# Kernel optimization log

Hardware: AMD Instinct MI355X
Metric: run time of the kernel (lower is better)

## Reference

```python
import jax, jax.numpy as jnp
import numpy as np

# cfg constants (from init_kwargs)
RBF_START = 0.0
RBF_END = 10.0
RBF_STEPS = 32
ENERGY_SCALE = 1.0
EPS = 1e-10

L, R, E, F, P = 64, 4096, 32, 64, 8


def setup_inputs() -> dict:
    key = jax.random.key(0)
    ks = jax.random.split(key, 6)
    return {
        "lig_feat": jax.random.normal(ks[0], (L, E, F), dtype=jnp.float32),
        "rec_feat": jax.random.normal(ks[1], (R, E, F), dtype=jnp.float32),
        "lig_coords": jax.random.normal(ks[2], (P, L, 3), dtype=jnp.float32),
        "rec_coord": jax.random.normal(ks[3], (R, 3), dtype=jnp.float32),
        "weight": jax.random.normal(ks[4], (), dtype=jnp.float32),
        "bias": jax.random.normal(ks[5], (), dtype=jnp.float32),
    }


def reference(lig_feat, rec_feat, lig_coords, rec_coord, weight, bias):
    # attention coefficients: [L, R, E]
    atn = jnp.einsum('lef,ref->lre', lig_feat, rec_feat)
    mu = jnp.linspace(RBF_START, RBF_END, RBF_STEPS, dtype=jnp.float32)  # [E]
    sigma = (RBF_START - RBF_END) / RBF_STEPS

    def energy(lig_coord):  # lig_coord: [L, 3]
        # cdist_diff: eps added per-coordinate before sum, as in the torch code
        diff = lig_coord[:, None, :] - rec_coord[None, :, :]      # [L, R, 3]
        dists = jnp.sqrt(((diff * diff) + EPS).sum(-1))            # [L, R]
        z = (dists[..., None] - mu) / sigma                        # [L, R, E]
        rbfs = jnp.exp(-(z * z))
        return (atn * rbfs * ENERGY_SCALE).sum()

    Us = jax.vmap(energy)(lig_coords)  # [P]
    # ScaleOutput
    return Us * weight + bias
```

## Files before the change

### kernel.cpp

```cpp
#include <hip/hip_runtime.h>

#define NL 64
#define NR 4096
#define NE 32
#define NF 64
#define NP 8

#define DSCALE 3.8435917081166390f
#define MUSTEP 1.2398683f
#define EPS3   3e-10f

typedef _Float16 f16x8 __attribute__((ext_vector_type(8)));
typedef __fp16   h16x2 __attribute__((ext_vector_type(2)));
typedef float    f32x4 __attribute__((ext_vector_type(4)));

#define NBLK   2048
#define DS_TAB_BYTES (NL * NR * NP * 2)

__global__ __launch_bounds__(256)
void ff_dist(const float* __restrict__ lig_coords,
             const float* __restrict__ rec_coord,
             void* __restrict__ ws)
{
    const int tid = blockIdx.x * 256 + threadIdx.x;
    const int l = tid >> 12;
    const int r = tid & 4095;
    const float rx = rec_coord[r * 3 + 0];
    const float ry = rec_coord[r * 3 + 1];
    const float rz = rec_coord[r * 3 + 2];
    float d[NP];
#pragma unroll
    for (int p = 0; p < NP; ++p) {
        const float lx = lig_coords[(p * NL + l) * 3 + 0];
        const float ly = lig_coords[(p * NL + l) * 3 + 1];
        const float lz = lig_coords[(p * NL + l) * 3 + 2];
        const float dx = lx - rx, dy = ly - ry, dz = lz - rz;
        const float d2 = fmaf(dx, dx, fmaf(dy, dy, fmaf(dz, dz, EPS3)));
        d[p] = __builtin_amdgcn_sqrtf(d2) * DSCALE;
    }
    union { h16x2 h[4]; uint4 u; } pk;
#pragma unroll
    for (int q = 0; q < 4; ++q)
        pk.h[q] = __builtin_amdgcn_cvt_pkrtz(d[2 * q], d[2 * q + 1]);
    ((uint4*)ws)[tid] = pk.u;
}

__global__ __launch_bounds__(256, 4)
void ff_main(const float* __restrict__ lig_feat,
             const float* __restrict__ rec_feat,
             void* __restrict__ ws)
{
    __shared__ __align__(16) char recs[8192];
    __shared__ float wred[32];

    const int t    = threadIdx.x;
    const int bid  = blockIdx.x;
    const int rb   = bid & 255;
    const int eb   = bid >> 8;
    const int r0   = rb * 16;
    const int e0   = eb * 4;
    const int lane = t & 63;
    const int wv   = t >> 6;
    const int l0   = wv * 16;
    const int cn   = lane & 15;
    const int kg   = lane >> 4;

    const int srow = t >> 4, sf = (t & 15) * 4;
    const int swz = (8 * (t & 15)) ^ ((srow & 7) << 4);
#pragma unroll
    for (int e = 0; e < 4; ++e) {
        const float4 v = *(const float4*)&rec_feat[((r0 + srow) * NE + e0 + e) * NF + sf];
        union { h16x2 h[2]; uint2 u; } pk;
        pk.h[0] = __builtin_amdgcn_cvt_pkrtz(v.x, v.y);
        pk.h[1] = __builtin_amdgcn_cvt_pkrtz(v.z, v.w);
        *(uint2*)(recs + e * 2048 + srow * 128 + swz) = pk.u;
    }

    const uint4* dtab = (const uint4*)ws;
    float ds[4][NP];
#pragma unroll
    for (int reg = 0; reg < 4; ++reg) {
        union { uint4 u; _Float16 h[8]; } pk;
        pk.u = dtab[(l0 + kg * 4 + reg) * NR + r0 + cn];
#pragma unroll
        for (int p = 0; p < NP; ++p) ds[reg][p] = (float)pk.h[p];
    }

    __syncthreads();

    const int bsw = (cn & 7) << 4;
    const int b_row = cn * 128;
    const int b0o = b_row + ((kg * 16) ^ bsw);
    const int b1o = b_row + ((kg * 16 + 64) ^ bsw);
    const float* ligb = &lig_feat[((l0 + cn) * NE + e0) * NF + kg * 8];

    float U[NP];
#pragma unroll
    for (int p = 0; p < NP; ++p) U[p] = 0.f;

#pragma unroll
    for (int ee = 0; ee < 4; ++ee) {
        const float4 af0 = *(const float4*)(ligb + ee * NF + 0);
        const float4 af1 = *(const float4*)(ligb + ee * NF + 4);
        const float4 af2 = *(const float4*)(ligb + ee * NF + 32);
        const float4 af3 = *(const float4*)(ligb + ee * NF + 36);
        union { h16x2 h[4]; f16x8 v; } a0, a1;
        a0.h[0] = __builtin_amdgcn_cvt_pkrtz(af0.x, af0.y);
        a0.h[1] = __builtin_amdgcn_cvt_pkrtz(af0.z, af0.w);
        a0.h[2] = __builtin_amdgcn_cvt_pkrtz(af1.x, af1.y);
        a0.h[3] = __builtin_amdgcn_cvt_pkrtz(af1.z, af1.w);
        a1.h[0] = __builtin_amdgcn_cvt_pkrtz(af2.x, af2.y);
        a1.h[1] = __builtin_amdgcn_cvt_pkrtz(af2.z, af2.w);
        a1.h[2] = __builtin_amdgcn_cvt_pkrtz(af3.x, af3.y);
        a1.h[3] = __builtin_amdgcn_cvt_pkrtz(af3.z, af3.w);
        const f16x8 b0 = *(const f16x8*)(recs + ee * 2048 + b0o);
        const f16x8 b1 = *(const f16x8*)(recs + ee * 2048 + b1o);
        f32x4 C = {0.f, 0.f, 0.f, 0.f};
        C = __builtin_amdgcn_mfma_f32_16x16x32_f16(a0.v, b0, C, 0, 0, 0);
        C = __builtin_amdgcn_mfma_f32_16x16x32_f16(a1.v, b1, C, 0, 0, 0);

        const float mu = (float)(e0 + ee) * MUSTEP;
#pragma unroll
        for (int reg = 0; reg < 4; ++reg) {
            const float a = C[reg];
#pragma unroll
            for (int p = 0; p < NP; ++p) {
                const float z = ds[reg][p] - mu;
                U[p] = fmaf(a, __builtin_amdgcn_exp2f(-(z * z)), U[p]);
            }
        }
    }

#pragma unroll
    for (int p = 0; p < NP; ++p) {
        float v = U[p];
        for (int off = 32; off; off >>= 1) v += __shfl_down(v, off, 64);
        U[p] = v;
    }
    __syncthreads();
    if (lane == 0) {
#pragma unroll
        for (int p = 0; p < NP; ++p) wred[wv * 8 + p] = U[p];
    }
    __syncthreads();
    float* wsP = (float*)((char*)ws + DS_TAB_BYTES);
    if (t < NP)
        wsP[t * NBLK + bid] = wred[t] + wred[8 + t] + wred[16 + t] + wred[24 + t];
}

__global__ __launch_bounds__(512)
void ff_fin(const void* __restrict__ ws,
            const float* __restrict__ w,
            const float* __restrict__ b,
            float* __restrict__ out) {
    const float* wsP = (const float*)((const char*)ws + DS_TAB_BYTES);
    const int t = threadIdx.x, lane = t & 63, p = t >> 6;
    float s = 0.f;
#pragma unroll
    for (int j = 0; j < NBLK / 256; ++j) {
        const float4 v = *(const float4*)&wsP[p * NBLK + j * 256 + lane * 4];
        s += (v.x + v.y) + (v.z + v.w);
    }
    for (int off = 32; off; off >>= 1) s += __shfl_down(s, off, 64);
    if (lane == 0) out[p] = fmaf(s, w[0], b[0]);
}

extern "C" void kernel_launch(void* const* d_in, const int* in_sizes, int n_in,
                              void* d_out, int out_size, void* d_ws, size_t ws_size,
                              hipStream_t stream) {
    const float* lig_feat   = (const float*)d_in[0];
    const float* rec_feat   = (const float*)d_in[1];
    const float* lig_coords = (const float*)d_in[2];
    const float* rec_coord  = (const float*)d_in[3];
    const float* weight     = (const float*)d_in[4];
    const float* bias       = (const float*)d_in[5];
    float* out = (float*)d_out;

    hipLaunchKernelGGL(ff_dist, dim3(1024), dim3(256), 0, stream,
                       lig_coords, rec_coord, d_ws);
    hipLaunchKernelGGL(ff_main, dim3(NBLK), dim3(256), 0, stream,
                       lig_feat, rec_feat, d_ws);
    hipLaunchKernelGGL(ff_fin, dim3(1), dim3(512), 0, stream,
                       d_ws, weight, bias, out);
}
```

Measured before the change: 33.85 us.

## Fuse distance computation into main kernel and double per-block embedding tile

Removes the separate distance-table kernel. Each main block now computes its own 64x16x8 half-precision distance tile in shared memory from ligand coordinates staged in LDS and receptor coordinates read from global memory. Each block also covers 8 embedding channels instead of 4, which halves the grid to 1024 blocks and the number of times the distance tile is recomputed. This removes one launch and the 4 MB global round trip of the distance table, at the cost of redundant sqrt work per block and more shared memory, about 40 KB, which may limit occupancy.

```diff
diff --git a/kernel.cpp b/kernel.cpp
--- a/kernel.cpp
+++ b/kernel.cpp
@@ -14,84 +14,95 @@
 typedef __fp16   h16x2 __attribute__((ext_vector_type(2)));
 typedef float    f32x4 __attribute__((ext_vector_type(4)));
 
-#define NBLK   2048
-#define DS_TAB_BYTES (NL * NR * NP * 2)
+#define NBLK 1024
 
-__global__ __launch_bounds__(256)
-void ff_dist(const float* __restrict__ lig_coords,
-             const float* __restrict__ rec_coord,
-             void* __restrict__ ws)
-{
-    const int tid = blockIdx.x * 256 + threadIdx.x;
-    const int l = tid >> 12;
-    const int r = tid & 4095;
-    const float rx = rec_coord[r * 3 + 0];
-    const float ry = rec_coord[r * 3 + 1];
-    const float rz = rec_coord[r * 3 + 2];
-    float d[NP];
-#pragma unroll
-    for (int p = 0; p < NP; ++p) {
-        const float lx = lig_coords[(p * NL + l) * 3 + 0];
-        const float ly = lig_coords[(p * NL + l) * 3 + 1];
-        const float lz = lig_coords[(p * NL + l) * 3 + 2];
-        const float dx = lx - rx, dy = ly - ry, dz = lz - rz;
-        const float d2 = fmaf(dx, dx, fmaf(dy, dy, fmaf(dz, dz, EPS3)));
-        d[p] = __builtin_amdgcn_sqrtf(d2) * DSCALE;
-    }
-    union { h16x2 h[4]; uint4 u; } pk;
-#pragma unroll
-    for (int q = 0; q < 4; ++q)
-        pk.h[q] = __builtin_amdgcn_cvt_pkrtz(d[2 * q], d[2 * q + 1]);
-    ((uint4*)ws)[tid] = pk.u;
-}
+#define COORD_B 0
+#define DTAB_B  8192
+#define REC_B   24576
 
 __global__ __launch_bounds__(256, 4)
 void ff_main(const float* __restrict__ lig_feat,
              const float* __restrict__ rec_feat,
-             void* __restrict__ ws)
+             const float* __restrict__ lig_coords,
+             const float* __restrict__ rec_coord,
+             float* __restrict__ ws)
 {
-    __shared__ __align__(16) char recs[8192];
-    __shared__ float wred[32];
+    __shared__ __align__(16) char smem[40960];
 
     const int t    = threadIdx.x;
     const int bid  = blockIdx.x;
     const int rb   = bid & 255;
     const int eb   = bid >> 8;
     const int r0   = rb * 16;
-    const int e0   = eb * 4;
+    const int e0   = eb * 8;
     const int lane = t & 63;
     const int wv   = t >> 6;
     const int l0   = wv * 16;
     const int cn   = lane & 15;
     const int kg   = lane >> 4;
 
-    const int srow = t >> 4, sf = (t & 15) * 4;
-    const int swz = (8 * (t & 15)) ^ ((srow & 7) << 4);
 #pragma unroll
-    for (int e = 0; e < 4; ++e) {
-        const float4 v = *(const float4*)&rec_feat[((r0 + srow) * NE + e0 + e) * NF + sf];
+    for (int j = 0; j < 6; ++j) {
+        const int s = j * 256 + t;
+        const int p = s / 192;
+        const int rem = s - p * 192;
+        const int l = rem / 3, c = rem - l * 3;
+        *(float*)(smem + COORD_B + (l * 8 + p) * 16 + c * 4) = lig_coords[s];
+    }
+    const int srow = t >> 4, sfq = t & 15;
+    const int rswz = (8 * sfq) ^ ((srow & 7) << 4);
+#pragma unroll
+    for (int e = 0; e < 8; ++e) {
+        const float4 v = *(const float4*)&rec_feat[((r0 + srow) * NE + e0 + e) * NF + sfq * 4];
         union { h16x2 h[2]; uint2 u; } pk;
         pk.h[0] = __builtin_amdgcn_cvt_pkrtz(v.x, v.y);
         pk.h[1] = __builtin_amdgcn_cvt_pkrtz(v.z, v.w);
-        *(uint2*)(recs + e * 2048 + srow * 128 + swz) = pk.u;
+        *(uint2*)(smem + REC_B + e * 2048 + srow * 128 + rswz) = pk.u;
     }
+    __syncthreads();
 
-    const uint4* dtab = (const uint4*)ws;
+    {
+        const int bl = t >> 2;
+        const int br = t & 3;
+        float4 lp[NP];
+#pragma unroll
+        for (int p = 0; p < NP; ++p)
+            lp[p] = *(const float4*)(smem + COORD_B + (bl * 8 + p) * 16);
+#pragma unroll
+        for (int j = 0; j < 4; ++j) {
+            const int r = br + 4 * j;
+            const float rx = rec_coord[(r0 + r) * 3 + 0];
+            const float ry = rec_coord[(r0 + r) * 3 + 1];
+            const float rz = rec_coord[(r0 + r) * 3 + 2];
+            float d[NP];
+#pragma unroll
+            for (int p = 0; p < NP; ++p) {
+                const float dx = lp[p].x - rx, dy = lp[p].y - ry, dz = lp[p].z - rz;
+                const float d2 = fmaf(dx, dx, fmaf(dy, dy, fmaf(dz, dz, EPS3)));
+                d[p] = __builtin_amdgcn_sqrtf(d2) * DSCALE;
+            }
+            union { h16x2 h[4]; uint4 u; } pk;
+#pragma unroll
+            for (int q = 0; q < 4; ++q)
+                pk.h[q] = __builtin_amdgcn_cvt_pkrtz(d[2 * q], d[2 * q + 1]);
+            *(uint4*)(smem + DTAB_B + bl * 256 + ((r * 16) ^ ((bl & 7) * 16))) = pk.u;
+        }
+    }
+    __syncthreads();
+
     float ds[4][NP];
 #pragma unroll
     for (int reg = 0; reg < 4; ++reg) {
+        const int l = l0 + kg * 4 + reg;
         union { uint4 u; _Float16 h[8]; } pk;
-        pk.u = dtab[(l0 + kg * 4 + reg) * NR + r0 + cn];
+        pk.u = *(const uint4*)(smem + DTAB_B + l * 256 + ((cn * 16) ^ ((l & 7) * 16)));
 #pragma unroll
         for (int p = 0; p < NP; ++p) ds[reg][p] = (float)pk.h[p];
     }
 
-    __syncthreads();
-
     const int bsw = (cn & 7) << 4;
-    const int b_row = cn * 128;
-    const int b0o = b_row + ((kg * 16) ^ bsw);
-    const int b1o = b_row + ((kg * 16 + 64) ^ bsw);
+    const int b0o = REC_B + cn * 128 + ((kg * 16) ^ bsw);
+    const int b1o = REC_B + cn * 128 + ((kg * 16 + 64) ^ bsw);
     const float* ligb = &lig_feat[((l0 + cn) * NE + e0) * NF + kg * 8];
 
     float U[NP];
@@ -99,7 +110,7 @@
     for (int p = 0; p < NP; ++p) U[p] = 0.f;
 
 #pragma unroll
-    for (int ee = 0; ee < 4; ++ee) {
+    for (int ee = 0; ee < 8; ++ee) {
         const float4 af0 = *(const float4*)(ligb + ee * NF + 0);
         const float4 af1 = *(const float4*)(ligb + ee * NF + 4);
         const float4 af2 = *(const float4*)(ligb + ee * NF + 32);
@@ -113,8 +124,8 @@
         a1.h[1] = __builtin_amdgcn_cvt_pkrtz(af2.z, af2.w);
         a1.h[2] = __builtin_amdgcn_cvt_pkrtz(af3.x, af3.y);
         a1.h[3] = __builtin_amdgcn_cvt_pkrtz(af3.z, af3.w);
-        const f16x8 b0 = *(const f16x8*)(recs + ee * 2048 + b0o);
-        const f16x8 b1 = *(const f16x8*)(recs + ee * 2048 + b1o);
+        const f16x8 b0 = *(const f16x8*)(smem + b0o + ee * 2048);
+        const f16x8 b1 = *(const f16x8*)(smem + b1o + ee * 2048);
         f32x4 C = {0.f, 0.f, 0.f, 0.f};
         C = __builtin_amdgcn_mfma_f32_16x16x32_f16(a0.v, b0, C, 0, 0, 0);
         C = __builtin_amdgcn_mfma_f32_16x16x32_f16(a1.v, b1, C, 0, 0, 0);
@@ -137,28 +148,26 @@
         for (int off = 32; off; off >>= 1) v += __shfl_down(v, off, 64);
         U[p] = v;
     }
-    __syncthreads();
+    float* wred = (float*)(smem + COORD_B);
     if (lane == 0) {
 #pragma unroll
         for (int p = 0; p < NP; ++p) wred[wv * 8 + p] = U[p];
     }
     __syncthreads();
-    float* wsP = (float*)((char*)ws + DS_TAB_BYTES);
     if (t < NP)
-        wsP[t * NBLK + bid] = wred[t] + wred[8 + t] + wred[16 + t] + wred[24 + t];
+        ws[t * NBLK + bid] = wred[t] + wred[8 + t] + wred[16 + t] + wred[24 + t];
 }
 
 __global__ __launch_bounds__(512)
-void ff_fin(const void* __restrict__ ws,
+void ff_fin(const float* __restrict__ ws,
             const float* __restrict__ w,
             const float* __restrict__ b,
             float* __restrict__ out) {
-    const float* wsP = (const float*)((const char*)ws + DS_TAB_BYTES);
     const int t = threadIdx.x, lane = t & 63, p = t >> 6;
     float s = 0.f;
 #pragma unroll
     for (int j = 0; j < NBLK / 256; ++j) {
-        const float4 v = *(const float4*)&wsP[p * NBLK + j * 256 + lane * 4];
+        const float4 v = *(const float4*)&ws[p * NBLK + j * 256 + lane * 4];
         s += (v.x + v.y) + (v.z + v.w);
     }
     for (int off = 32; off; off >>= 1) s += __shfl_down(s, off, 64);
@@ -175,11 +184,10 @@
     const float* weight     = (const float*)d_in[4];
     const float* bias       = (const float*)d_in[5];
     float* out = (float*)d_out;
+    float* ws  = (float*)d_ws;
 
-    hipLaunchKernelGGL(ff_dist, dim3(1024), dim3(256), 0, stream,
-                       lig_coords, rec_coord, d_ws);
     hipLaunchKernelGGL(ff_main, dim3(NBLK), dim3(256), 0, stream,
-                       lig_feat, rec_feat, d_ws);
+                       lig_feat, rec_feat, lig_coords, rec_coord, ws);
     hipLaunchKernelGGL(ff_fin, dim3(1), dim3(512), 0, stream,
-                       d_ws, weight, bias, out);
+                       ws, weight, bias, out);
 }
```

Result: faster. 29.41 us (-13.1%).
